# Kernel optimization log

Hardware: AMD Instinct MI355X
Metric: run time of the kernel (lower is better)

Reference implementation:

```python
import jax, jax.numpy as jnp
import numpy as np

B, N, DIM = 32, 576, 1024
H, HD = 16, 64            # head_dim = DIM // H
M = HD * 2                # rand_feat_dim = head_dim * rand_feat_dim_ratio(2) = 128
LAM = 0.1
NUM_STEP = 10
SCALE = HD ** (-0.5)


def setup_inputs() -> dict:
    key = jax.random.key(0)
    ks = jax.random.split(key, 6)
    x = jax.random.normal(ks[0], (B, N, DIM), dtype=jnp.float32)
    qkv_w = jax.random.normal(ks[1], (2 * DIM, DIM), dtype=jnp.float32) * 0.02
    proj_w = jax.random.normal(ks[2], (DIM, DIM), dtype=jnp.float32) * 0.02
    proj_b = jnp.zeros((DIM,), dtype=jnp.float32)
    rand_matrix = jax.random.normal(ks[3], (H, HD, M), dtype=jnp.float32)
    kernel = jax.random.normal(ks[4], (1, H, N, M), dtype=jnp.float32)
    learned_k = jnp.eye(2 * M, dtype=jnp.float32)
    learned_lam = jnp.ones((1,), dtype=jnp.float32)
    learned_L = jnp.ones((1,), dtype=jnp.float32)
    return {"x": x, "qkv_w": qkv_w, "proj_w": proj_w, "proj_b": proj_b,
            "rand_matrix": rand_matrix, "kernel": kernel,
            "learned_k": learned_k, "learned_lam": learned_lam,
            "learned_L": learned_L}


def _soft_thresh(z, t):
    # torch: sign(z) * GELU(|z| - t), exact (erf) GELU
    return jnp.sign(z) * jax.nn.gelu(jnp.abs(z) - t, approximate=False)


def reference(x, qkv_w, proj_w, proj_b, rand_matrix, kernel,
              learned_k, learned_lam, learned_L):
    # qkv projection (no bias), split into q and v heads: [B,H,N,HD]
    qkv = (x @ qkv_w.T).reshape(B, N, 2, H, HD)
    q = jnp.transpose(qkv[:, :, 0], (0, 2, 1, 3))
    v = jnp.transpose(qkv[:, :, 1], (0, 2, 1, 3))

    # random-feature map (Performer-style positive features)
    q = q * SCALE ** 0.5
    logits = jnp.einsum('bhnd,hdm->bhnm', q, rand_matrix)
    sqnorm = 0.5 * jnp.sum(q * q, axis=-1, keepdims=True)
    phi = jnp.exp(logits - sqnorm) / (M ** 0.5)                 # [B,H,N,M]

    # concat learned kernel features, L2-normalize over token dim (dim=-2)
    q = jnp.concatenate([phi, jnp.broadcast_to(kernel, (B, H, N, M))], axis=-1)
    nrm = jnp.linalg.norm(q, axis=-2, keepdims=True)
    q = q / jnp.maximum(nrm, 1e-12)                              # [B,H,N,2M]

    kk = jnp.einsum('bhnp,bhnq->bhpq', q, q)                     # [B,H,2M,2M]
    inp = jnp.einsum('bhnp,bhnd->bhpd', q, v)                    # [B,H,2M,HD]

    # ISTA-like unrolled solver
    L = jax.lax.stop_gradient(
        jnp.max(jnp.sum(jnp.abs(kk), axis=-1), axis=-1))[..., None, None] + 1.0
    lam_learned = learned_lam * LAM                              # [1]
    eff_L = L / learned_L                                        # [B,H,1,1]
    kk_learned = jnp.einsum('pq,bhqr,rs->bhps', learned_k, kk, learned_k)

    z = _soft_thresh(inp, lam_learned)
    for _ in range(NUM_STEP):
        z = z - (jnp.einsum('bhpq,bhqd->bhpd', kk_learned, z) - inp) / eff_L
        z = _soft_thresh(z, lam_learned / eff_L)

    out = jnp.einsum('bhnp,bhpd->bhnd', q, z)                    # [B,H,N,HD]
    out = jnp.transpose(out, (0, 2, 1, 3)).reshape(B, N, DIM)
    return out @ proj_w.T + proj_b
```

## Files before the change

### kernel.cpp

```cpp
#include <hip/hip_runtime.h>
#include <math.h>

#define NN 576
#define LAMC 0.1f
#define NUM_STEP 10

typedef unsigned short u16;
typedef __attribute__((ext_vector_type(8))) short bf16x8;
typedef __attribute__((ext_vector_type(4))) float f32x4;

__device__ __forceinline__ float bf2f(u16 u) { return __uint_as_float(((unsigned)u) << 16); }
__device__ __forceinline__ u16 f2bf(float f) {
    unsigned x = __float_as_uint(f);
    return (u16)((x + 0x7fffu + ((x >> 16) & 1u)) >> 16);
}
__device__ __forceinline__ float soft_thresh(float z, float t) {
    float a = fabsf(z) - t;
    float g = 0.5f * a * (1.0f + erff(a * 0.70710678118654752f));
    float s = (z > 0.0f) ? 1.0f : ((z < 0.0f) ? -1.0f : 0.0f);
    return s * g;
}
__device__ __forceinline__ void gload16(const u16* g, const u16* l) {
    __builtin_amdgcn_global_load_lds(
        (const __attribute__((address_space(1))) unsigned int*)(g),
        (__attribute__((address_space(3))) unsigned int*)(l), 16, 0, 0);
}

__global__ __launch_bounds__(256) void k_cvt(const float* __restrict__ in,
                                             u16* __restrict__ out, int n4) {
    const int i = blockIdx.x * 256 + threadIdx.x;
    if (i >= n4) return;
    float4 v = reinterpret_cast<const float4*>(in)[i];
    ushort4 o;
    o.x = f2bf(v.x); o.y = f2bf(v.y); o.z = f2bf(v.z); o.w = f2bf(v.w);
    reinterpret_cast<ushort4*>(out)[i] = o;
}

__global__ __launch_bounds__(256) void k_cvtT(const float* __restrict__ Lk,
                                              u16* __restrict__ LkT) {
    const int r = blockIdx.x, s = threadIdx.x;
    LkT[r * 256 + s] = f2bf(Lk[s * 256 + r]);
}

__global__ __launch_bounds__(256) void k_randT(const float* __restrict__ rand_m,
                                               u16* __restrict__ randT) {
    const int i = blockIdx.x * 256 + threadIdx.x;
    const int h = i >> 13, rem = i & 8191;
    const int m = rem >> 6, d = rem & 63;
    randT[i] = f2bf(rand_m[(size_t)h * 8192 + d * 128 + m]);
}

__device__ __forceinline__ void nt128_body(const u16* __restrict__ A, const u16* __restrict__ B,
                                           const int K, u16 (&As)[128][32], u16 (&Bs)[128][32],
                                           f32x4 (&acc)[4][4]) {
    const int tid = threadIdx.x;
    const int lane = tid & 63, wid = tid >> 6;
    const int wr = (wid >> 1) * 64, wc = (wid & 1) * 64;
    const int fr = lane & 15, kg = lane >> 4;
    for (int k0 = 0; k0 < K; k0 += 32) {
        __syncthreads();
        #pragma unroll
        for (int c = 0; c < 2; ++c) {
            const int ch = wid + c * 4;
            gload16(&A[(size_t)(ch * 16 + (lane >> 2)) * K + k0 + (lane & 3) * 8], &As[ch * 16][0]);
            gload16(&B[(size_t)(ch * 16 + (lane >> 2)) * K + k0 + (lane & 3) * 8], &Bs[ch * 16][0]);
        }
        __syncthreads();
        bf16x8 af[4], bfr[4];
        #pragma unroll
        for (int i = 0; i < 4; ++i) af[i] = *reinterpret_cast<const bf16x8*>(&As[wr + i * 16 + fr][kg * 8]);
        #pragma unroll
        for (int j = 0; j < 4; ++j) bfr[j] = *reinterpret_cast<const bf16x8*>(&Bs[wc + j * 16 + fr][kg * 8]);
        #pragma unroll
        for (int i = 0; i < 4; ++i)
            #pragma unroll
            for (int j = 0; j < 4; ++j)
                acc[i][j] = __builtin_amdgcn_mfma_f32_16x16x32_bf16(af[i], bfr[j], acc[i][j], 0, 0, 0);
    }
}

__device__ __forceinline__ void store_c_bf16(u16* __restrict__ C, f32x4 (&acc)[4][4]) {
    const int tid = threadIdx.x;
    const int lane = tid & 63, wid = tid >> 6;
    const int wr = (wid >> 1) * 64, wc = (wid & 1) * 64;
    const int fr = lane & 15, kg = lane >> 4;
    #pragma unroll
    for (int i = 0; i < 4; ++i)
        #pragma unroll
        for (int r = 0; r < 4; ++r)
            #pragma unroll
            for (int j = 0; j < 4; ++j)
                C[(size_t)(wr + i * 16 + kg * 4 + r) * 256 + wc + j * 16 + fr] = f2bf(acc[i][j][r]);
}

__global__ __launch_bounds__(256) void k_qkv_mfma(const u16* __restrict__ A,
                                                  const u16* __restrict__ B,
                                                  u16* __restrict__ qbf,
                                                  u16* __restrict__ vT) {
    __shared__ u16 As[128][32];
    __shared__ u16 Bs[128][32];
    const int tid = threadIdx.x;
    const int wid = tid >> 6, lane = tid & 63;
    const int wr = (wid >> 1) * 64, wc = (wid & 1) * 64;
    const int lb = (blockIdx.x & 7) * 288 + (blockIdx.x >> 3);
    const int bm = lb >> 4, bn = lb & 15;
    const int row0 = bm * 128, col0 = bn * 128;
    const int fr = lane & 15, kg = lane >> 4;
    f32x4 acc[4][4];
    #pragma unroll
    for (int i = 0; i < 4; ++i)
        #pragma unroll
        for (int j = 0; j < 4; ++j) acc[i][j] = (f32x4){0.f, 0.f, 0.f, 0.f};
    nt128_body(A + (size_t)row0 * 1024, B + (size_t)col0 * 1024, 1024, As, Bs, acc);
    const bool isQ = (col0 < 1024);
    if (isQ) {
        const float qscale = 0.35355339059327373f;
        #pragma unroll
        for (int i = 0; i < 4; ++i) {
            #pragma unroll
            for (int r = 0; r < 4; ++r) {
                const int grow = row0 + wr + i * 16 + kg * 4 + r;
                const int b = grow / NN, n = grow % NN;
                #pragma unroll
                for (int j = 0; j < 4; ++j) {
                    const int gcol = col0 + wc + j * 16 + fr;
                    const int h = gcol >> 6, d = gcol & 63;
                    qbf[(((size_t)b * 16 + h) * NN + n) * 64 + d] = f2bf(acc[i][j][r] * qscale);
                }
            }
        }
    } else {
        #pragma unroll
        for (int i = 0; i < 4; ++i) {
            const int gb = row0 + wr + i * 16 + kg * 4;
            const int b = gb / NN, n = gb % NN;
            #pragma unroll
            for (int j = 0; j < 4; ++j) {
                const int c2 = col0 + wc + j * 16 + fr - 1024;
                const int h = c2 >> 6, d = c2 & 63;
                ushort4 pk;
                pk.x = f2bf(acc[i][j][0]); pk.y = f2bf(acc[i][j][1]);
                pk.z = f2bf(acc[i][j][2]); pk.w = f2bf(acc[i][j][3]);
                *reinterpret_cast<ushort4*>(&vT[(((size_t)b * 16 + h) * 64 + d) * 576 + n]) = pk;
            }
        }
    }
}

__global__ __launch_bounds__(256) void k_phi_mfma(const u16* __restrict__ qbf,
                                                  const u16* __restrict__ randT,
                                                  u16* __restrict__ phiT) {
    __shared__ u16 Rs[128][72];
    __shared__ u16 Qs[64][72];
    __shared__ u16 Ph[128][72];
    __shared__ float sn[64];
    __shared__ float snorm[256];
    const int bh = blockIdx.x, h = bh & 15;
    const int tid = threadIdx.x, lane = tid & 63, wid = tid >> 6;
    const int fr = lane & 15, kg = lane >> 4;
    #pragma unroll
    for (int c = 0; c < 4; ++c) {
        const int i = c * 256 + tid;
        const int m = i >> 3, k8 = (i & 7) * 8;
        *reinterpret_cast<uint4*>(&Rs[m][k8]) =
            *reinterpret_cast<const uint4*>(&randT[((size_t)h * 128 + m) * 64 + k8]);
    }
    const u16* Q = qbf + (size_t)bh * 576 * 64;
    const float invM = 0.08838834764831845f;
    for (int nc = 0; nc < 9; ++nc) {
        const int n0 = nc * 64;
        __syncthreads();
        #pragma unroll
        for (int c = 0; c < 2; ++c) {
            const int i = c * 256 + tid;
            const int r = i >> 3, k8 = (i & 7) * 8;
            *reinterpret_cast<uint4*>(&Qs[r][k8]) =
                *reinterpret_cast<const uint4*>(&Q[(size_t)(n0 + r) * 64 + k8]);
        }
        __syncthreads();
        if (tid < 64) {
            float s = 0.f;
            #pragma unroll 8
            for (int d = 0; d < 64; ++d) { float v = bf2f(Qs[tid][d]); s = fmaf(v, v, s); }
            sn[tid] = 0.5f * s;
        }
        f32x4 acc[2][4];
        #pragma unroll
        for (int i = 0; i < 2; ++i)
            #pragma unroll
            for (int j = 0; j < 4; ++j) acc[i][j] = (f32x4){0.f, 0.f, 0.f, 0.f};
        #pragma unroll
        for (int ks = 0; ks < 2; ++ks) {
            bf16x8 af[2], bq[4];
            #pragma unroll
            for (int i = 0; i < 2; ++i)
                af[i] = *reinterpret_cast<const bf16x8*>(&Rs[wid * 32 + i * 16 + fr][ks * 32 + kg * 8]);
            #pragma unroll
            for (int j = 0; j < 4; ++j)
                bq[j] = *reinterpret_cast<const bf16x8*>(&Qs[j * 16 + fr][ks * 32 + kg * 8]);
            #pragma unroll
            for (int i = 0; i < 2; ++i)
                #pragma unroll
                for (int j = 0; j < 4; ++j)
                    acc[i][j] = __builtin_amdgcn_mfma_f32_16x16x32_bf16(af[i], bq[j], acc[i][j], 0, 0, 0);
        }
        __syncthreads();
        #pragma unroll
        for (int j = 0; j < 4; ++j) {
            const int n = j * 16 + fr;
            const float sv = sn[n];
            #pragma unroll
            for (int i = 0; i < 2; ++i) {
                #pragma unroll
                for (int r = 0; r < 4; ++r) {
                    const int m = wid * 32 + i * 16 + kg * 4 + r;
                    Ph[m][n] = f2bf(expf(acc[i][j][r] - sv) * invM);
                }
            }
        }
        __syncthreads();
        #pragma unroll
        for (int c = 0; c < 4; ++c) {
            const int i = c * 256 + tid;
            const int mm = i >> 3, k8 = (i & 7) * 8;
            *reinterpret_cast<uint4*>(&phiT[((size_t)bh * 128 + mm) * 576 + n0 + k8]) =
                *reinterpret_cast<const uint4*>(&Ph[mm][k8]);
        }
    }
    __syncthreads();
    {
        const int m = tid & 127, half = tid >> 7;
        u16* row = phiT + ((size_t)bh * 128 + m) * 576 + half * 288;
        float s = 0.f;
        for (int n = 0; n < 288; n += 8) {
            uint4 v = *reinterpret_cast<const uint4*>(&row[n]);
            float f0 = __uint_as_float(v.x << 16), f1 = __uint_as_float(v.x & 0xffff0000u);
            float f2 = __uint_as_float(v.y << 16), f3 = __uint_as_float(v.y & 0xffff0000u);
            float f4 = __uint_as_float(v.z << 16), f5 = __uint_as_float(v.z & 0xffff0000u);
            float f6 = __uint_as_float(v.w << 16), f7 = __uint_as_float(v.w & 0xffff0000u);
            s += f0*f0 + f1*f1 + f2*f2 + f3*f3 + f4*f4 + f5*f5 + f6*f6 + f7*f7;
        }
        snorm[tid] = s;
        __syncthreads();
        const float inv = 1.0f / fmaxf(sqrtf(snorm[m] + snorm[128 + m]), 1e-12f);
        for (int n = 0; n < 288; n += 8) {
            uint4 v = *reinterpret_cast<const uint4*>(&row[n]);
            uint4 o;
            o.x = (unsigned)f2bf(__uint_as_float(v.x << 16) * inv) |
                  ((unsigned)f2bf(__uint_as_float(v.x & 0xffff0000u) * inv) << 16);
            o.y = (unsigned)f2bf(__uint_as_float(v.y << 16) * inv) |
                  ((unsigned)f2bf(__uint_as_float(v.y & 0xffff0000u) * inv) << 16);
            o.z = (unsigned)f2bf(__uint_as_float(v.z << 16) * inv) |
                  ((unsigned)f2bf(__uint_as_float(v.z & 0xffff0000u) * inv) << 16);
            o.w = (unsigned)f2bf(__uint_as_float(v.w << 16) * inv) |
                  ((unsigned)f2bf(__uint_as_float(v.w & 0xffff0000u) * inv) << 16);
            *reinterpret_cast<uint4*>(&row[n]) = o;
        }
    }
}

__global__ __launch_bounds__(128) void k_kernormT(const float* __restrict__ kern,
                                                  u16* __restrict__ kerT) {
    const int h = blockIdx.x, m = threadIdx.x;
    const float* kp = kern + (size_t)h * NN * 128 + m;
    float s = 0.f;
    for (int n = 0; n < NN; ++n) { float v = kp[(size_t)n * 128]; s = fmaf(v, v, s); }
    const float inv = 1.0f / fmaxf(sqrtf(s), 1e-12f);
    u16* op = kerT + ((size_t)h * 128 + m) * 576;
    for (int n = 0; n < NN; ++n) op[n] = f2bf(kp[(size_t)n * 128] * inv);
}

__global__ __launch_bounds__(256) void k_gram_mfma(const u16* __restrict__ phiT,
                                                   const u16* __restrict__ kerT,
                                                   u16* __restrict__ kkb) {
    __shared__ u16 As[128][32];
    __shared__ u16 Bs[128][32];
    const int lb = (blockIdx.x & 7) * 256 + (blockIdx.x >> 3);
    const int bh = lb >> 2, bm = (lb >> 1) & 1, bn = lb & 1;
    const int h = bh & 15;
    const u16* A = bm ? kerT + (size_t)h * 73728 : phiT + (size_t)bh * 73728;
    const u16* B = bn ? kerT + (size_t)h * 73728 : phiT + (size_t)bh * 73728;
    f32x4 acc[4][4];
    #pragma unroll
    for (int i = 0; i < 4; ++i)
        #pragma unroll
        for (int j = 0; j < 4; ++j) acc[i][j] = (f32x4){0.f, 0.f, 0.f, 0.f};
    nt128_body(A, B, 576, As, Bs, acc);
    store_c_bf16(kkb + (size_t)bh * 65536 + bm * 128 * 256 + bn * 128, acc);
}

__global__ __launch_bounds__(256) void k_lk_mfma(const u16* __restrict__ Ab, size_t sA,
                                                 const u16* __restrict__ Bb, size_t sB,
                                                 u16* __restrict__ Cb) {
    __shared__ u16 As[128][32];
    __shared__ u16 Bs[128][32];
    const int lb = (blockIdx.x & 7) * 256 + (blockIdx.x >> 3);
    const int idx = lb >> 2, bm = (lb >> 1) & 1, bn = lb & 1;
    const u16* A = Ab + (size_t)idx * sA + bm * 128 * 256;
    const u16* B = Bb + (size_t)idx * sB + bn * 128 * 256;
    f32x4 acc[4][4];
    #pragma unroll
    for (int i = 0; i < 4; ++i)
        #pragma unroll
        for (int j = 0; j < 4; ++j) acc[i][j] = (f32x4){0.f, 0.f, 0.f, 0.f};
    nt128_body(A, B, 256, As, Bs, acc);
    store_c_bf16(Cb + (size_t)idx * 65536 + bm * 128 * 256 + bn * 128, acc);
}

__global__ __launch_bounds__(256) void k_inp_mfma(const u16* __restrict__ vT,
                                                  const u16* __restrict__ phiT,
                                                  const u16* __restrict__ kerT,
                                                  float* __restrict__ inpT) {
    __shared__ u16 As[64][40];
    __shared__ u16 Bs[256][40];
    const int bh = blockIdx.x, h = bh & 15;
    const int tid = threadIdx.x, lane = tid & 63, wid = tid >> 6;
    const int fr = lane & 15, kg = lane >> 4;
    const u16* Av = vT + (size_t)bh * 64 * 576;
    f32x4 acc[4][4];
    #pragma unroll
    for (int i = 0; i < 4; ++i)
        #pragma unroll
        for (int j = 0; j < 4; ++j) acc[i][j] = (f32x4){0.f, 0.f, 0.f, 0.f};
    for (int k0 = 0; k0 < 576; k0 += 32) {
        __syncthreads();
        { const int r = tid >> 2, k8 = (tid & 3) * 8;
          *reinterpret_cast<uint4*>(&As[r][k8]) =
              *reinterpret_cast<const uint4*>(&Av[(size_t)r * 576 + k0 + k8]); }
        #pragma unroll
        for (int c = 0; c < 4; ++c) {
            const int q = c * 256 + tid;
            const int r = q >> 2, k8 = (q & 3) * 8;
            const u16* src = (r < 128) ? phiT + ((size_t)bh * 128 + r) * 576
                                       : kerT + ((size_t)h * 128 + (r - 128)) * 576;
            *reinterpret_cast<uint4*>(&Bs[r][k8]) =
                *reinterpret_cast<const uint4*>(&src[k0 + k8]);
        }
        __syncthreads();
        bf16x8 af[4], bfr[4];
        #pragma unroll
        for (int i = 0; i < 4; ++i) af[i] = *reinterpret_cast<const bf16x8*>(&As[i * 16 + fr][kg * 8]);
        #pragma unroll
        for (int j = 0; j < 4; ++j) bfr[j] = *reinterpret_cast<const bf16x8*>(&Bs[wid * 64 + j * 16 + fr][kg * 8]);
        #pragma unroll
        for (int i = 0; i < 4; ++i)
            #pragma unroll
            for (int j = 0; j < 4; ++j)
                acc[i][j] = __builtin_amdgcn_mfma_f32_16x16x32_bf16(af[i], bfr[j], acc[i][j], 0, 0, 0);
    }
    float* O = inpT + (size_t)bh * 16384;
    #pragma unroll
    for (int i = 0; i < 4; ++i)
        #pragma unroll
        for (int r = 0; r < 4; ++r)
            #pragma unroll
            for (int j = 0; j < 4; ++j)
                O[(size_t)(i * 16 + kg * 4 + r) * 256 + wid * 64 + j * 16 + fr] = acc[i][j][r];
}

__global__ __launch_bounds__(256) void k_L(const u16* __restrict__ kkb,
                                           const float* __restrict__ lL,
                                           float* __restrict__ effL) {
    const int bh = blockIdx.x;
    const u16* row = kkb + (size_t)bh * 65536 + (size_t)threadIdx.x * 256;
    float s = 0.f;
    for (int q = 0; q < 256; ++q) s += fabsf(bf2f(row[q]));
    __shared__ float red[256];
    red[threadIdx.x] = s;
    __syncthreads();
    for (int st = 128; st > 0; st >>= 1) {
        if (threadIdx.x < st) red[threadIdx.x] = fmaxf(red[threadIdx.x], red[threadIdx.x + st]);
        __syncthreads();
    }
    if (threadIdx.x == 0) effL[bh] = (red[0] + 1.0f) / lL[0];
}

__global__ __launch_bounds__(256) void k_ista_reg(const u16* __restrict__ kkl,
                                                  const float* __restrict__ inpT,
                                                  u16* __restrict__ zbf,
                                                  const float* __restrict__ effL,
                                                  const float* __restrict__ llam) {
    __shared__ u16 zs[32][256];
    const int bh = blockIdx.x >> 1, dh = blockIdx.x & 1;
    const int tid = threadIdx.x, lane = tid & 63, wid = tid >> 6;
    const int wr = wid * 64;
    const int fr = lane & 15, kg = lane >> 4;
    const u16* Kk = kkl + (size_t)bh * 65536;
    bf16x8 af[4][8];
    #pragma unroll
    for (int i = 0; i < 4; ++i) {
        const int p = wr + i * 16 + fr;
        #pragma unroll
        for (int c = 0; c < 8; ++c)
            af[i][c] = *reinterpret_cast<const bf16x8*>(&Kk[(size_t)p * 256 + c * 32 + kg * 8]);
    }
    const float* I = inpT + (size_t)bh * 16384 + (size_t)dh * 32 * 256;
    const float invL = 1.0f / effL[bh];
    const float lam = llam[0] * LAMC;
    const float thr = lam * invL;
    float4 ip[4][2];
    #pragma unroll
    for (int i = 0; i < 4; ++i) {
        const int pb = wr + i * 16 + kg * 4;
        #pragma unroll
        for (int j = 0; j < 2; ++j) {
            const int d = j * 16 + fr;
            ip[i][j] = *reinterpret_cast<const float4*>(&I[(size_t)d * 256 + pb]);
            const int pc = pb ^ ((d & 7) << 3);
            ushort4 pk;
            pk.x = f2bf(soft_thresh(ip[i][j].x, lam));
            pk.y = f2bf(soft_thresh(ip[i][j].y, lam));
            pk.z = f2bf(soft_thresh(ip[i][j].z, lam));
            pk.w = f2bf(soft_thresh(ip[i][j].w, lam));
            *reinterpret_cast<ushort4*>(&zs[d][pc]) = pk;
        }
    }
    __syncthreads();
    for (int step = 0; step < NUM_STEP; ++step) {
        f32x4 acc[4][2];
        #pragma unroll
        for (int i = 0; i < 4; ++i)
            #pragma unroll
            for (int j = 0; j < 2; ++j) acc[i][j] = (f32x4){0.f, 0.f, 0.f, 0.f};
        #pragma unroll
        for (int c = 0; c < 8; ++c) {
            bf16x8 bz[2];
            #pragma unroll
            for (int j = 0; j < 2; ++j) {
                const int d = j * 16 + fr;
                bz[j] = *reinterpret_cast<const bf16x8*>(&zs[d][(c * 32 + kg * 8) ^ ((d & 7) << 3)]);
            }
            #pragma unroll
            for (int i = 0; i < 4; ++i)
                #pragma unroll
                for (int j = 0; j < 2; ++j)
                    acc[i][j] = __builtin_amdgcn_mfma_f32_16x16x32_bf16(af[i][c], bz[j], acc[i][j], 0, 0, 0);
        }
        __syncthreads();
        #pragma unroll
        for (int i = 0; i < 4; ++i) {
            const int pb = wr + i * 16 + kg * 4;
            #pragma unroll
            for (int j = 0; j < 2; ++j) {
                const int d = j * 16 + fr;
                const int pc = pb ^ ((d & 7) << 3);
                ushort4 zo = *reinterpret_cast<const ushort4*>(&zs[d][pc]);
                ushort4 pk;
                pk.x = f2bf(soft_thresh(bf2f(zo.x) - (acc[i][j][0] - ip[i][j].x) * invL, thr));
                pk.y = f2bf(soft_thresh(bf2f(zo.y) - (acc[i][j][1] - ip[i][j].y) * invL, thr));
                pk.z = f2bf(soft_thresh(bf2f(zo.z) - (acc[i][j][2] - ip[i][j].z) * invL, thr));
                pk.w = f2bf(soft_thresh(bf2f(zo.w) - (acc[i][j][3] - ip[i][j].w) * invL, thr));
                *reinterpret_cast<ushort4*>(&zs[d][pc]) = pk;
            }
        }
        __syncthreads();
    }
    u16* Z = zbf + (size_t)bh * 16384 + (size_t)dh * 32 * 256;
    #pragma unroll
    for (int c = 0; c < 4; ++c) {
        const int i = c * 256 + tid;
        const int d = i >> 5, p8 = (i & 31) * 8;
        *reinterpret_cast<uint4*>(&Z[(size_t)d * 256 + p8]) =
            *reinterpret_cast<const uint4*>(&zs[d][p8 ^ ((d & 7) << 3)]);
    }
}

__global__ __launch_bounds__(256) void k_outpre_mfma(const u16* __restrict__ phiT,
                                                     const u16* __restrict__ kerT,
                                                     const u16* __restrict__ zbf,
                                                     u16* __restrict__ outp) {
    __shared__ u16 Zs[64][264];
    __shared__ u16 Qt[64][264];
    __shared__ u16 Os[64][72];
    const int bh = blockIdx.x, b = bh >> 4, h = bh & 15;
    const int tid = threadIdx.x, lane = tid & 63, wid = tid >> 6;
    const int fr = lane & 15, kg = lane >> 4;
    const u16* Z = zbf + (size_t)bh * 16384;
    #pragma unroll
    for (int c = 0; c < 8; ++c) {
        const int i = c * 256 + tid;
        const int d = i >> 5, k8 = (i & 31) * 8;
        *reinterpret_cast<uint4*>(&Zs[d][k8]) =
            *reinterpret_cast<const uint4*>(&Z[(size_t)d * 256 + k8]);
    }
    for (int nc = 0; nc < 9; ++nc) {
        const int n0 = nc * 64;
        __syncthreads();
        #pragma unroll
        for (int c = 0; c < 8; ++c) {
            const int i = c * 256 + tid;
            const int p = i >> 3, j8 = (i & 7) * 8;
            const u16* src = (p < 128) ? &phiT[((size_t)bh * 128 + p) * 576 + n0 + j8]
                                       : &kerT[((size_t)h * 128 + (p - 128)) * 576 + n0 + j8];
            uint4 v = *reinterpret_cast<const uint4*>(src);
            Qt[j8 + 0][p] = (u16)(v.x & 0xffffu); Qt[j8 + 1][p] = (u16)(v.x >> 16);
            Qt[j8 + 2][p] = (u16)(v.y & 0xffffu); Qt[j8 + 3][p] = (u16)(v.y >> 16);
            Qt[j8 + 4][p] = (u16)(v.z & 0xffffu); Qt[j8 + 5][p] = (u16)(v.z >> 16);
            Qt[j8 + 6][p] = (u16)(v.w & 0xffffu); Qt[j8 + 7][p] = (u16)(v.w >> 16);
        }
        __syncthreads();
        f32x4 acc[4];
        #pragma unroll
        for (int j = 0; j < 4; ++j) acc[j] = (f32x4){0.f, 0.f, 0.f, 0.f};
        #pragma unroll
        for (int ks = 0; ks < 8; ++ks) {
            bf16x8 aq = *reinterpret_cast<const bf16x8*>(&Qt[wid * 16 + fr][ks * 32 + kg * 8]);
            #pragma unroll
            for (int j = 0; j < 4; ++j) {
                bf16x8 bz = *reinterpret_cast<const bf16x8*>(&Zs[j * 16 + fr][ks * 32 + kg * 8]);
                acc[j] = __builtin_amdgcn_mfma_f32_16x16x32_bf16(aq, bz, acc[j], 0, 0, 0);
            }
        }
        __syncthreads();
        #pragma unroll
        for (int j = 0; j < 4; ++j)
            #pragma unroll
            for (int r = 0; r < 4; ++r)
                Os[wid * 16 + kg * 4 + r][j * 16 + fr] = f2bf(acc[j][r]);
        __syncthreads();
        #pragma unroll
        for (int c = 0; c < 2; ++c) {
            const int i = c * 256 + tid;
            const int nn = i >> 3, k8 = (i & 7) * 8;
            *reinterpret_cast<uint4*>(&outp[((size_t)b * NN + n0 + nn) * 1024 + h * 64 + k8]) =
                *reinterpret_cast<const uint4*>(&Os[nn][k8]);
        }
    }
}

__global__ __launch_bounds__(256) void k_proj_mfma(const u16* __restrict__ A,
                                                   const u16* __restrict__ B,
                                                   const float* __restrict__ bias,
                                                   float* __restrict__ out) {
    __shared__ u16 As[128][32];
    __shared__ u16 Bs[128][32];
    const int tid = threadIdx.x;
    const int wid = tid >> 6, lane = tid & 63;
    const int wr = (wid >> 1) * 64, wc = (wid & 1) * 64;
    const int lb = (blockIdx.x & 7) * 144 + (blockIdx.x >> 3);
    const int bm = lb >> 3, bn = lb & 7;
    const int row0 = bm * 128, col0 = bn * 128;
    const int fr = lane & 15, kg = lane >> 4;
    f32x4 acc[4][4];
    #pragma unroll
    for (int i = 0; i < 4; ++i)
        #pragma unroll
        for (int j = 0; j < 4; ++j) acc[i][j] = (f32x4){0.f, 0.f, 0.f, 0.f};
    nt128_body(A + (size_t)row0 * 1024, B + (size_t)col0 * 1024, 1024, As, Bs, acc);
    #pragma unroll
    for (int i = 0; i < 4; ++i)
        #pragma unroll
        for (int r = 0; r < 4; ++r) {
            const int grow = row0 + wr + i * 16 + kg * 4 + r;
            #pragma unroll
            for (int j = 0; j < 4; ++j) {
                const int gcol = col0 + wc + j * 16 + fr;
                out[(size_t)grow * 1024 + gcol] = acc[i][j][r] + bias[gcol];
            }
        }
}

extern "C" void kernel_launch(void* const* d_in, const int* in_sizes, int n_in,
                              void* d_out, int out_size, void* d_ws, size_t ws_size,
                              hipStream_t stream) {
    const float* x      = (const float*)d_in[0];
    const float* qkv_w  = (const float*)d_in[1];
    const float* proj_w = (const float*)d_in[2];
    const float* proj_b = (const float*)d_in[3];
    const float* rand_m = (const float*)d_in[4];
    const float* kern   = (const float*)d_in[5];
    const float* Lk     = (const float*)d_in[6];
    const float* llam   = (const float*)d_in[7];
    const float* lL     = (const float*)d_in[8];
    float* out = (float*)d_out;

    const size_t NEED = 248252416ull;
    if (ws_size < NEED) { hipMemsetAsync(d_out, 0, (size_t)out_size * 4, stream); return; }
    char* base = (char*)d_ws;
    u16*   pwb  = (u16*)  (base + 0);
    float* effL = (float*)(base + 2097152);
    u16*   Lkb  = (u16*)  (base + 2099200);
    u16*   LkTb = (u16*)  (base + 2230272);
    u16*   kerT = (u16*)  (base + 2361344);
    u16*   randT= (u16*)  (base + 4720640);
    u16*   phiT = (u16*)  (base + 4982784);
    u16*   kkb  = (u16*)  (base + 80480256);
    float* inpT = (float*)(base + 147589120);
    u16*   zbf  = (u16*)  (base + 181143552);
    u16*   vT   = (u16*)  (base + 80480256);
    u16*   wb   = (u16*)  (base + 118228992);
    u16*   qbf  = (u16*)  (base + 147589120);
    u16*   xb   = (u16*)  (base + 197920768);
    u16*   tmpb = (u16*)  (base + 181143552);
    u16*   outp = (u16*)  (base + 80480256);

    k_cvt        <<<18432, 256, 0, stream>>>(x, xb, 4718592);
    k_cvt        <<<2048,  256, 0, stream>>>(qkv_w, wb, 524288);
    k_cvt        <<<1024,  256, 0, stream>>>(proj_w, pwb, 262144);
    k_cvt        <<<64,    256, 0, stream>>>(Lk, Lkb, 16384);
    k_cvtT       <<<256,   256, 0, stream>>>(Lk, LkTb);
    k_randT      <<<512,   256, 0, stream>>>(rand_m, randT);
    k_kernormT   <<<16,    128, 0, stream>>>(kern, kerT);
    k_qkv_mfma   <<<2304,  256, 0, stream>>>(xb, wb, qbf, vT);
    k_phi_mfma   <<<512,   256, 0, stream>>>(qbf, randT, phiT);
    k_inp_mfma   <<<512,   256, 0, stream>>>(vT, phiT, kerT, inpT);
    k_gram_mfma  <<<2048,  256, 0, stream>>>(phiT, kerT, kkb);
    k_L          <<<512,   256, 0, stream>>>(kkb, lL, effL);
    k_lk_mfma    <<<2048,  256, 0, stream>>>(Lkb, 0, kkb, 65536, tmpb);
    k_lk_mfma    <<<2048,  256, 0, stream>>>(tmpb, 65536, LkTb, 0, kkb);
    k_ista_reg   <<<1024,  256, 0, stream>>>(kkb, inpT, zbf, effL, llam);
    k_outpre_mfma<<<512,   256, 0, stream>>>(phiT, kerT, zbf, outp);
    k_proj_mfma  <<<1152,  256, 0, stream>>>(outp, pwb, proj_b, out);
}
```

Baseline: 695.7 us.

## Defer phi column normalization into consumer kernels via per-feature inverse norms

The phi kernel no longer re-reads and rewrites phiT to normalize it. It accumulates squared norms from shared memory as tiles are produced and stores one inverse norm per feature row. The gram, inp and outpre kernels then apply these scales in their epilogues or when loading Z. This removes a second global read/write pass over phiT at the cost of extra scaling work in three consumers, and it changes where bf16 rounding happens.

After: 626.3 us. 1.11x faster.

```diff
diff --git a/kernel.cpp b/kernel.cpp
--- a/kernel.cpp
+++ b/kernel.cpp
@@ -149,7 +149,8 @@
 
 __global__ __launch_bounds__(256) void k_phi_mfma(const u16* __restrict__ qbf,
                                                   const u16* __restrict__ randT,
-                                                  u16* __restrict__ phiT) {
+                                                  u16* __restrict__ phiT,
+                                                  float* __restrict__ invn) {
     __shared__ u16 Rs[128][72];
     __shared__ u16 Qs[64][72];
     __shared__ u16 Ph[128][72];
@@ -167,6 +168,8 @@
     }
     const u16* Q = qbf + (size_t)bh * 576 * 64;
     const float invM = 0.08838834764831845f;
+    float accs = 0.f;
+    const int m2 = tid >> 1, c0 = (tid & 1) * 32;
     for (int nc = 0; nc < 9; ++nc) {
         const int n0 = nc * 64;
         __syncthreads();
@@ -226,37 +229,17 @@
             *reinterpret_cast<uint4*>(&phiT[((size_t)bh * 128 + mm) * 576 + n0 + k8]) =
                 *reinterpret_cast<const uint4*>(&Ph[mm][k8]);
         }
-    }
+        {
+            float s = 0.f;
+            #pragma unroll 8
+            for (int t = 0; t < 32; ++t) { float v = bf2f(Ph[m2][c0 + t]); s = fmaf(v, v, s); }
+            accs += s;
+        }
+    }
+    snorm[tid] = accs;
     __syncthreads();
-    {
-        const int m = tid & 127, half = tid >> 7;
-        u16* row = phiT + ((size_t)bh * 128 + m) * 576 + half * 288;
-        float s = 0.f;
-        for (int n = 0; n < 288; n += 8) {
-            uint4 v = *reinterpret_cast<const uint4*>(&row[n]);
-            float f0 = __uint_as_float(v.x << 16), f1 = __uint_as_float(v.x & 0xffff0000u);
-            float f2 = __uint_as_float(v.y << 16), f3 = __uint_as_float(v.y & 0xffff0000u);
-            float f4 = __uint_as_float(v.z << 16), f5 = __uint_as_float(v.z & 0xffff0000u);
-            float f6 = __uint_as_float(v.w << 16), f7 = __uint_as_float(v.w & 0xffff0000u);
-            s += f0*f0 + f1*f1 + f2*f2 + f3*f3 + f4*f4 + f5*f5 + f6*f6 + f7*f7;
-        }
-        snorm[tid] = s;
-        __syncthreads();
-        const float inv = 1.0f / fmaxf(sqrtf(snorm[m] + snorm[128 + m]), 1e-12f);
-        for (int n = 0; n < 288; n += 8) {
-            uint4 v = *reinterpret_cast<const uint4*>(&row[n]);
-            uint4 o;
-            o.x = (unsigned)f2bf(__uint_as_float(v.x << 16) * inv) |
-                  ((unsigned)f2bf(__uint_as_float(v.x & 0xffff0000u) * inv) << 16);
-            o.y = (unsigned)f2bf(__uint_as_float(v.y << 16) * inv) |
-                  ((unsigned)f2bf(__uint_as_float(v.y & 0xffff0000u) * inv) << 16);
-            o.z = (unsigned)f2bf(__uint_as_float(v.z << 16) * inv) |
-                  ((unsigned)f2bf(__uint_as_float(v.z & 0xffff0000u) * inv) << 16);
-            o.w = (unsigned)f2bf(__uint_as_float(v.w << 16) * inv) |
-                  ((unsigned)f2bf(__uint_as_float(v.w & 0xffff0000u) * inv) << 16);
-            *reinterpret_cast<uint4*>(&row[n]) = o;
-        }
-    }
+    if (tid < 128)
+        invn[bh * 128 + tid] = 1.0f / fmaxf(sqrtf(snorm[tid * 2] + snorm[tid * 2 + 1]), 1e-12f);
 }
 
 __global__ __launch_bounds__(128) void k_kernormT(const float* __restrict__ kern,
@@ -272,6 +255,7 @@
 
 __global__ __launch_bounds__(256) void k_gram_mfma(const u16* __restrict__ phiT,
                                                    const u16* __restrict__ kerT,
+                                                   const float* __restrict__ invn,
                                                    u16* __restrict__ kkb) {
     __shared__ u16 As[128][32];
     __shared__ u16 Bs[128][32];
@@ -286,7 +270,24 @@
         #pragma unroll
         for (int j = 0; j < 4; ++j) acc[i][j] = (f32x4){0.f, 0.f, 0.f, 0.f};
     nt128_body(A, B, 576, As, Bs, acc);
-    store_c_bf16(kkb + (size_t)bh * 65536 + bm * 128 * 256 + bn * 128, acc);
+    const int tid = threadIdx.x, lane = tid & 63, wid = tid >> 6;
+    const int wr = (wid >> 1) * 64, wc = (wid & 1) * 64;
+    const int fr = lane & 15, kg = lane >> 4;
+    const float* iv = invn + bh * 128;
+    u16* C = kkb + (size_t)bh * 65536 + bm * 128 * 256 + bn * 128;
+    float sq[4];
+    #pragma unroll
+    for (int j = 0; j < 4; ++j) sq[j] = bn ? 1.0f : iv[wc + j * 16 + fr];
+    #pragma unroll
+    for (int i = 0; i < 4; ++i)
+        #pragma unroll
+        for (int r = 0; r < 4; ++r) {
+            const int p = wr + i * 16 + kg * 4 + r;
+            const float sp = bm ? 1.0f : iv[p];
+            #pragma unroll
+            for (int j = 0; j < 4; ++j)
+                C[(size_t)p * 256 + wc + j * 16 + fr] = f2bf(acc[i][j][r] * sp * sq[j]);
+        }
 }
 
 __global__ __launch_bounds__(256) void k_lk_mfma(const u16* __restrict__ Ab, size_t sA,
@@ -310,6 +311,7 @@
 __global__ __launch_bounds__(256) void k_inp_mfma(const u16* __restrict__ vT,
                                                   const u16* __restrict__ phiT,
                                                   const u16* __restrict__ kerT,
+                                                  const float* __restrict__ invn,
                                                   float* __restrict__ inpT) {
     __shared__ u16 As[64][40];
     __shared__ u16 Bs[256][40];
@@ -349,13 +351,19 @@
                 acc[i][j] = __builtin_amdgcn_mfma_f32_16x16x32_bf16(af[i], bfr[j], acc[i][j], 0, 0, 0);
     }
     float* O = inpT + (size_t)bh * 16384;
+    float sc[4];
+    #pragma unroll
+    for (int j = 0; j < 4; ++j) {
+        const int p = wid * 64 + j * 16 + fr;
+        sc[j] = (p < 128) ? invn[bh * 128 + p] : 1.0f;
+    }
     #pragma unroll
     for (int i = 0; i < 4; ++i)
         #pragma unroll
         for (int r = 0; r < 4; ++r)
             #pragma unroll
             for (int j = 0; j < 4; ++j)
-                O[(size_t)(i * 16 + kg * 4 + r) * 256 + wid * 64 + j * 16 + fr] = acc[i][j][r];
+                O[(size_t)(i * 16 + kg * 4 + r) * 256 + wid * 64 + j * 16 + fr] = acc[i][j][r] * sc[j];
 }
 
 __global__ __launch_bounds__(256) void k_L(const u16* __restrict__ kkb,
@@ -468,6 +476,7 @@
 __global__ __launch_bounds__(256) void k_outpre_mfma(const u16* __restrict__ phiT,
                                                      const u16* __restrict__ kerT,
                                                      const u16* __restrict__ zbf,
+                                                     const float* __restrict__ invn,
                                                      u16* __restrict__ outp) {
     __shared__ u16 Zs[64][264];
     __shared__ u16 Qt[64][264];
@@ -480,8 +489,22 @@
     for (int c = 0; c < 8; ++c) {
         const int i = c * 256 + tid;
         const int d = i >> 5, k8 = (i & 31) * 8;
-        *reinterpret_cast<uint4*>(&Zs[d][k8]) =
-            *reinterpret_cast<const uint4*>(&Z[(size_t)d * 256 + k8]);
+        uint4 v = *reinterpret_cast<const uint4*>(&Z[(size_t)d * 256 + k8]);
+        if (k8 < 128) {
+            const float4 s0 = *reinterpret_cast<const float4*>(&invn[bh * 128 + k8]);
+            const float4 s1 = *reinterpret_cast<const float4*>(&invn[bh * 128 + k8 + 4]);
+            uint4 o;
+            o.x = (unsigned)f2bf(__uint_as_float(v.x << 16) * s0.x) |
+                  ((unsigned)f2bf(__uint_as_float(v.x & 0xffff0000u) * s0.y) << 16);
+            o.y = (unsigned)f2bf(__uint_as_float(v.y << 16) * s0.z) |
+                  ((unsigned)f2bf(__uint_as_float(v.y & 0xffff0000u) * s0.w) << 16);
+            o.z = (unsigned)f2bf(__uint_as_float(v.z << 16) * s1.x) |
+                  ((unsigned)f2bf(__uint_as_float(v.z & 0xffff0000u) * s1.y) << 16);
+            o.w = (unsigned)f2bf(__uint_as_float(v.w << 16) * s1.z) |
+                  ((unsigned)f2bf(__uint_as_float(v.w & 0xffff0000u) * s1.w) << 16);
+            v = o;
+        }
+        *reinterpret_cast<uint4*>(&Zs[d][k8]) = v;
     }
     for (int nc = 0; nc < 9; ++nc) {
         const int n0 = nc * 64;
@@ -574,7 +597,7 @@
     const float* lL     = (const float*)d_in[8];
     float* out = (float*)d_out;
 
-    const size_t NEED = 248252416ull;
+    const size_t NEED = 248514560ull;
     if (ws_size < NEED) { hipMemsetAsync(d_out, 0, (size_t)out_size * 4, stream); return; }
     char* base = (char*)d_ws;
     u16*   pwb  = (u16*)  (base + 0);
@@ -587,6 +610,7 @@
     u16*   kkb  = (u16*)  (base + 80480256);
     float* inpT = (float*)(base + 147589120);
     u16*   zbf  = (u16*)  (base + 181143552);
+    float* invn = (float*)(base + 248252416);
     u16*   vT   = (u16*)  (base + 80480256);
     u16*   wb   = (u16*)  (base + 118228992);
     u16*   qbf  = (u16*)  (base + 147589120);
@@ -602,13 +626,13 @@
     k_randT      <<<512,   256, 0, stream>>>(rand_m, randT);
     k_kernormT   <<<16,    128, 0, stream>>>(kern, kerT);
     k_qkv_mfma   <<<2304,  256, 0, stream>>>(xb, wb, qbf, vT);
-    k_phi_mfma   <<<512,   256, 0, stream>>>(qbf, randT, phiT);
-    k_inp_mfma   <<<512,   256, 0, stream>>>(vT, phiT, kerT, inpT);
-    k_gram_mfma  <<<2048,  256, 0, stream>>>(phiT, kerT, kkb);
+    k_phi_mfma   <<<512,   256, 0, stream>>>(qbf, randT, phiT, invn);
+    k_inp_mfma   <<<512,   256, 0, stream>>>(vT, phiT, kerT, invn, inpT);
+    k_gram_mfma  <<<2048,  256, 0, stream>>>(phiT, kerT, invn, kkb);
     k_L          <<<512,   256, 0, stream>>>(kkb, lL, effL);
     k_lk_mfma    <<<2048,  256, 0, stream>>>(Lkb, 0, kkb, 65536, tmpb);
     k_lk_mfma    <<<2048,  256, 0, stream>>>(tmpb, 65536, LkTb, 0, kkb);
     k_ista_reg   <<<1024,  256, 0, stream>>>(kkb, inpT, zbf, effL, llam);
-    k_outpre_mfma<<<512,   256, 0, stream>>>(phiT, kerT, zbf, outp);
+    k_outpre_mfma<<<512,   256, 0, stream>>>(phiT, kerT, zbf, invn, outp);
     k_proj_mfma  <<<1152,  256, 0, stream>>>(outp, pwb, proj_b, out);
 }
```
